# Optimization experiments

Hardware: AMD Instinct MI355X
Metric: run time of the kernel (lower is better)

The kernel has to match this reference:

```python
import jax, jax.numpy as jnp
import numpy as np

B, S, E = 2, 2048, 1024
H, NQ = 16, 8          # n_heads, n_qubits
D = E // H             # head_dim


def setup_inputs() -> dict:
    key = jax.random.key(0)
    ks = jax.random.split(key, 11)
    sc = 0.02
    return {
        "query": jax.random.normal(ks[0], (B, S, E), jnp.float32),
        "key":   jax.random.normal(ks[1], (B, S, E), jnp.float32),
        "value": jax.random.normal(ks[2], (B, S, E), jnp.float32),
        "Wq": jax.random.normal(ks[3], (E, NQ), jnp.float32) * sc,
        "bq": jnp.zeros((NQ,), jnp.float32),
        "Wk": jax.random.normal(ks[4], (E, NQ), jnp.float32) * sc,
        "bk": jnp.zeros((NQ,), jnp.float32),
        "Wv": jax.random.normal(ks[5], (E, E), jnp.float32) * sc,
        "bv": jnp.zeros((E,), jnp.float32),
        "Wo": jax.random.normal(ks[6], (E, E), jnp.float32) * sc,
        "bo": jnp.zeros((E,), jnp.float32),
    }


def reference(query, key, value, Wq, bq, Wk, bk, Wv, bv, Wo, bo):
    # Linear encoders (q/k are computed in the original but, because
    # _apply_rotation is the identity, they never influence the scores).
    q = query @ Wq + bq            # [B,S,NQ] (dead math, kept for fidelity)
    k = key @ Wk + bk              # [B,S,NQ]
    v = value @ Wv + bv            # [B,S,E]
    v = v.reshape(B, S, H, D).transpose(0, 2, 1, 3)  # [B,H,S,D]

    # Quantum overlap: both encoded states are always |0>, so
    # |<q_state|k_state>|^2 == 1 for every (b,i,j) pair.
    scores = jnp.full((B, H, S, S), 1.0 / np.sqrt(NQ), dtype=query.dtype)
    attn = jax.nn.softmax(scores, axis=-1)           # uniform 1/S weights

    out = jnp.einsum('bhij,bhjd->bhid', attn, v)     # [B,H,S,D]
    out = out.transpose(0, 2, 1, 3).reshape(B, S, E)
    out = out @ Wo + bo
    return out, attn
```

## Files before the change

kernel.cpp:

```cpp
#include <hip/hip_runtime.h>


typedef float floatx4 __attribute__((ext_vector_type(4)));

#define ATTN_BASE4 1048576LL
#define K1_FILLB   2512
#define K2_FILLB   2960
#define K3_FILLB   2720

__device__ __forceinline__ void fill_at(float* __restrict__ out, long long f4base) {
    floatx4* o4 = (floatx4*)out;
    const floatx4 av = (floatx4)(1.0f / 2048.0f);
    long long base = f4base + threadIdx.x;
    #pragma unroll
    for (int it = 0; it < 16; ++it)
        __builtin_nontemporal_store(av, &o4[base + it * 256]);
}

__global__ void __launch_bounds__(256)
k1_colsum_fill(const float* __restrict__ value,
               float* __restrict__ part1,
               float* __restrict__ out) {
    int blk = blockIdx.x, t = threadIdx.x;
    if (blk < 256) {
        int b = blk >> 7, sp = blk & 127;
        const floatx4* v4 = (const floatx4*)value;
        floatx4 acc = (floatx4)0.0f;
        int rowbase = b * 2048 + sp * 16;
        #pragma unroll
        for (int r = 0; r < 16; ++r)
            acc += v4[(size_t)(rowbase + r) * 256 + t];
        ((floatx4*)part1)[(size_t)(b * 128 + sp) * 256 + t] = acc;
    } else {
        fill_at(out, ATTN_BASE4 + (long long)(blk - 256) * 4096);
    }
}

__global__ void __launch_bounds__(256)
k2_z_fill(const float* __restrict__ part1,
          const float* __restrict__ Wv, const float* __restrict__ bv,
          float* __restrict__ z,
          float* __restrict__ out) {
    int blk = blockIdx.x, t = threadIdx.x;
    if (blk < 128) {
        __shared__ __align__(16) float vbar[1024];
        __shared__ float red[256];
        int b = blk >> 6, grp = blk & 63, e0 = grp * 16;

        const floatx4* p4 = (const floatx4*)part1 + (size_t)b * 128 * 256;
        floatx4 acc = (floatx4)0.0f;
        #pragma unroll 8
        for (int sp = 0; sp < 128; ++sp)
            acc += p4[sp * 256 + t];
        ((floatx4*)vbar)[t] = acc * (1.0f / 2048.0f);
        __syncthreads();

        int col = t & 15, seg = t >> 4;
        const float* wcol = Wv + e0 + col;
        float part = 0.f;
        int k0 = seg * 64;
        #pragma unroll 8
        for (int kk = 0; kk < 64; ++kk) {
            int k = k0 + kk;
            part += vbar[k] * wcol[(size_t)k * 1024];
        }
        red[t] = part;
        __syncthreads();
        if (t < 16) {
            float s = bv[e0 + t];
            #pragma unroll
            for (int g = 0; g < 16; ++g) s += red[g * 16 + t];
            z[b * 1024 + e0 + t] = s;
        }
    } else {
        fill_at(out, ATTN_BASE4 + (long long)K1_FILLB * 4096
                     + (long long)(blk - 128) * 4096);
    }
}

__global__ void __launch_bounds__(256)
k3_orow_bcast_fill(const float* __restrict__ z,
                   const float* __restrict__ Wo, const float* __restrict__ bo,
                   float* __restrict__ out) {
    int blk = blockIdx.x, t = threadIdx.x;
    if (blk < 128) {
        __shared__ __align__(16) float zsh[1024];
        __shared__ float red[256];
        __shared__ __align__(16) float orow[16];
        int b = blk >> 6, grp = blk & 63, e0 = grp * 16;

        ((floatx4*)zsh)[t] = ((const floatx4*)z)[b * 256 + t];
        __syncthreads();

        int col = t & 15, seg = t >> 4;
        const float* wcol = Wo + e0 + col;
        float part = 0.f;
        int k0 = seg * 64;
        #pragma unroll 8
        for (int kk = 0; kk < 64; ++kk) {
            int k = k0 + kk;
            part += zsh[k] * wcol[(size_t)k * 1024];
        }
        red[t] = part;
        __syncthreads();
        if (t < 16) {
            float s = bo[e0 + t];
            #pragma unroll
            for (int g = 0; g < 16; ++g) s += red[g * 16 + t];
            orow[t] = s;
        }
        __syncthreads();

        int q = t & 3, rl = t >> 2;
        floatx4 w = ((const floatx4*)orow)[q];
        floatx4* o4 = (floatx4*)out;
        size_t cbase = (size_t)(e0 >> 2) + q;
        #pragma unroll 4
        for (int r = rl; r < 2048; r += 64)
            __builtin_nontemporal_store(w, &o4[((size_t)b * 2048 + r) * 256 + cbase]);
    } else {
        fill_at(out, ATTN_BASE4 + (long long)(K1_FILLB + K2_FILLB) * 4096
                     + (long long)(blk - 128) * 4096);
    }
}

extern "C" void kernel_launch(void* const* d_in, const int* in_sizes, int n_in,
                              void* d_out, int out_size, void* d_ws, size_t ws_size,
                              hipStream_t stream) {
    const float* value = (const float*)d_in[2];
    const float* Wv    = (const float*)d_in[7];
    const float* bv    = (const float*)d_in[8];
    const float* Wo    = (const float*)d_in[9];
    const float* bo    = (const float*)d_in[10];
    float* out = (float*)d_out;

    float* part1 = (float*)d_ws;
    float* zbuf  = part1 + 262144;

    k1_colsum_fill    <<<256 + K1_FILLB, 256, 0, stream>>>(value, part1, out);
    k2_z_fill         <<<128 + K2_FILLB, 256, 0, stream>>>(part1, Wv, bv, zbuf, out);
    k3_orow_bcast_fill<<<128 + K3_FILLB, 256, 0, stream>>>(zbuf, Wo, bo, out);
}
```

Before: 114.1 us.

## Split Wv GEMV into partial-sum stage and widen Wo broadcast across more blocks

The v-bar @ Wv product is now split over k-slices into partial sums with coalesced float2 row reads of Wv, followed by a small reduction kernel that adds the bias. The Wo stage and its row broadcast run on 1024 blocks instead of 128, and every kernel uses a fixed 2048-block grid whose remaining blocks loop over 4 KB chunks of the uniform attention fill. The aim is to raise parallelism on the critical GEMV chain and keep the fill work balanced across stages. The cost is an extra kernel launch, an extra workspace round-trip, and the Wo GEMV being recomputed eight times per column group.

```diff
diff --git a/kernel.cpp b/kernel.cpp
--- a/kernel.cpp
+++ b/kernel.cpp
@@ -2,25 +2,33 @@
 
 
 typedef float floatx4 __attribute__((ext_vector_type(4)));
+typedef float floatx2 __attribute__((ext_vector_type(2)));
 
 #define ATTN_BASE4 1048576LL
-#define K1_FILLB   2512
-#define K2_FILLB   2960
-#define K3_FILLB   2720
+#define O1 0
+#define F1 7168
+#define O2 7168
+#define F2 8800
+#define O3 15968
+#define F3 9380
+#define O4 25348
+#define F4 7420
 
-__device__ __forceinline__ void fill_at(float* __restrict__ out, long long f4base) {
+__device__ __forceinline__ void fill_chunks(float* __restrict__ out,
+                                            int fb, int nf, int O, int F) {
     floatx4* o4 = (floatx4*)out;
     const floatx4 av = (floatx4)(1.0f / 2048.0f);
-    long long base = f4base + threadIdx.x;
-    #pragma unroll
-    for (int it = 0; it < 16; ++it)
-        __builtin_nontemporal_store(av, &o4[base + it * 256]);
+    for (int c = fb; c < F; c += nf) {
+        long long base = ATTN_BASE4 + ((long long)(O + c) << 10) + threadIdx.x;
+        #pragma unroll
+        for (int it = 0; it < 4; ++it)
+            __builtin_nontemporal_store(av, &o4[base + it * 256]);
+    }
 }
 
 __global__ void __launch_bounds__(256)
 k1_colsum_fill(const float* __restrict__ value,
-               float* __restrict__ part1,
-               float* __restrict__ out) {
+               float* __restrict__ part1, float* __restrict__ out) {
     int blk = blockIdx.x, t = threadIdx.x;
     if (blk < 256) {
         int b = blk >> 7, sp = blk & 127;
@@ -32,95 +40,107 @@
             acc += v4[(size_t)(rowbase + r) * 256 + t];
         ((floatx4*)part1)[(size_t)(b * 128 + sp) * 256 + t] = acc;
     } else {
-        fill_at(out, ATTN_BASE4 + (long long)(blk - 256) * 4096);
+        fill_chunks(out, blk - 256, 1792, O1, F1);
     }
 }
 
 __global__ void __launch_bounds__(256)
-k2_z_fill(const float* __restrict__ part1,
-          const float* __restrict__ Wv, const float* __restrict__ bv,
-          float* __restrict__ z,
-          float* __restrict__ out) {
+k2_zpart_fill(const float* __restrict__ part1, const float* __restrict__ Wv,
+              float* __restrict__ zpart, float* __restrict__ out) {
     int blk = blockIdx.x, t = threadIdx.x;
     if (blk < 128) {
-        __shared__ __align__(16) float vbar[1024];
         __shared__ float red[256];
-        int b = blk >> 6, grp = blk & 63, e0 = grp * 16;
+        __shared__ float vsl[32];
+        int b = blk >> 6, r = blk & 63, ks = r >> 1, eh = r & 1;
+        int k0 = ks * 32;
+        int kl = t & 31, sg = t >> 5;
+        float s = 0.f;
+        #pragma unroll
+        for (int i = 0; i < 16; ++i) {
+            int sp = sg * 16 + i;
+            s += part1[(size_t)(b * 128 + sp) * 1024 + k0 + kl];
+        }
+        red[t] = s;
+        __syncthreads();
+        if (t < 32) {
+            float v = 0.f;
+            #pragma unroll
+            for (int g = 0; g < 8; ++g) v += red[g * 32 + t];
+            vsl[t] = v * (1.0f / 2048.0f);
+        }
+        __syncthreads();
+        int e2 = eh * 512 + 2 * t;
+        floatx2 acc = (floatx2)0.0f;
+        #pragma unroll 8
+        for (int kk = 0; kk < 32; ++kk) {
+            floatx2 w = *(const floatx2*)&Wv[(size_t)(k0 + kk) * 1024 + e2];
+            acc += vsl[kk] * w;
+        }
+        *(floatx2*)&zpart[(size_t)(b * 32 + ks) * 1024 + e2] = acc;
+    } else {
+        fill_chunks(out, blk - 128, 1920, O2, F2);
+    }
+}
 
-        const floatx4* p4 = (const floatx4*)part1 + (size_t)b * 128 * 256;
-        floatx4 acc = (floatx4)0.0f;
+__global__ void __launch_bounds__(256)
+k3_zfin_fill(const float* __restrict__ zpart, const float* __restrict__ bv,
+             float* __restrict__ z, float* __restrict__ out) {
+    int blk = blockIdx.x, t = threadIdx.x;
+    if (blk < 64) {
+        int b = blk >> 5, es = blk & 31, e0 = es * 32;
+        if (t < 32) {
+            float s = bv[e0 + t];
+            #pragma unroll 8
+            for (int seg = 0; seg < 32; ++seg)
+                s += zpart[(size_t)(b * 32 + seg) * 1024 + e0 + t];
+            z[b * 1024 + e0 + t] = s;
+        }
+    } else {
+        fill_chunks(out, blk - 64, 1984, O3, F3);
+    }
+}
+
+__global__ void __launch_bounds__(256)
+k4_orow_bcast_fill(const float* __restrict__ z, const float* __restrict__ Wo,
+                   const float* __restrict__ bo, float* __restrict__ out) {
+    int blk = blockIdx.x, t = threadIdx.x;
+    if (blk < 1024) {
+        __shared__ __align__(16) float zsh[1024];
+        __shared__ float red[256];
+        __shared__ __align__(16) float orow[16];
+        int b = blk >> 9, r = blk & 511, cg = r >> 3, rr = r & 7;
+        int e0 = cg * 16;
+        ((floatx4*)zsh)[t] = ((const floatx4*)z)[b * 256 + t];
+        __syncthreads();
+        int eo = e0 + (t & 15), sg = t >> 4;
+        float part = 0.f;
+        int eb = sg * 64;
         #pragma unroll 8
-        for (int sp = 0; sp < 128; ++sp)
-            acc += p4[sp * 256 + t];
-        ((floatx4*)vbar)[t] = acc * (1.0f / 2048.0f);
-        __syncthreads();
-
-        int col = t & 15, seg = t >> 4;
-        const float* wcol = Wv + e0 + col;
-        float part = 0.f;
-        int k0 = seg * 64;
-        #pragma unroll 8
-        for (int kk = 0; kk < 64; ++kk) {
-            int k = k0 + kk;
-            part += vbar[k] * wcol[(size_t)k * 1024];
+        for (int ee = 0; ee < 64; ++ee) {
+            int e = eb + ee;
+            part += zsh[e] * Wo[(size_t)e * 1024 + eo];
         }
         red[t] = part;
         __syncthreads();
         if (t < 16) {
-            float s = bv[e0 + t];
+            float o = bo[e0 + t];
             #pragma unroll
-            for (int g = 0; g < 16; ++g) s += red[g * 16 + t];
-            z[b * 1024 + e0 + t] = s;
-        }
-    } else {
-        fill_at(out, ATTN_BASE4 + (long long)K1_FILLB * 4096
-                     + (long long)(blk - 128) * 4096);
-    }
-}
-
-__global__ void __launch_bounds__(256)
-k3_orow_bcast_fill(const float* __restrict__ z,
-                   const float* __restrict__ Wo, const float* __restrict__ bo,
-                   float* __restrict__ out) {
-    int blk = blockIdx.x, t = threadIdx.x;
-    if (blk < 128) {
-        __shared__ __align__(16) float zsh[1024];
-        __shared__ float red[256];
-        __shared__ __align__(16) float orow[16];
-        int b = blk >> 6, grp = blk & 63, e0 = grp * 16;
-
-        ((floatx4*)zsh)[t] = ((const floatx4*)z)[b * 256 + t];
-        __syncthreads();
-
-        int col = t & 15, seg = t >> 4;
-        const float* wcol = Wo + e0 + col;
-        float part = 0.f;
-        int k0 = seg * 64;
-        #pragma unroll 8
-        for (int kk = 0; kk < 64; ++kk) {
-            int k = k0 + kk;
-            part += zsh[k] * wcol[(size_t)k * 1024];
-        }
-        red[t] = part;
-        __syncthreads();
-        if (t < 16) {
-            float s = bo[e0 + t];
-            #pragma unroll
-            for (int g = 0; g < 16; ++g) s += red[g * 16 + t];
-            orow[t] = s;
+            for (int g = 0; g < 16; ++g) o += red[g * 16 + t];
+            orow[t] = o;
         }
         __syncthreads();
-
         int q = t & 3, rl = t >> 2;
         floatx4 w = ((const floatx4*)orow)[q];
         floatx4* o4 = (floatx4*)out;
-        size_t cbase = (size_t)(e0 >> 2) + q;
-        #pragma unroll 4
-        for (int r = rl; r < 2048; r += 64)
-            __builtin_nontemporal_store(w, &o4[((size_t)b * 2048 + r) * 256 + cbase]);
+        size_t cb = (size_t)(e0 >> 2) + q;
+        int rbase = rr * 256;
+        #pragma unroll
+        for (int i = 0; i < 4; ++i) {
+            int row = rbase + i * 64 + rl;
+            __builtin_nontemporal_store(w, &o4[((size_t)b * 2048 + row) * 256 + cb]);
+        }
     } else {
-        fill_at(out, ATTN_BASE4 + (long long)(K1_FILLB + K2_FILLB) * 4096
-                     + (long long)(blk - 128) * 4096);
+        fill_chunks(out, blk - 1024, 1024, O4, F4);
     }
 }
 
@@ -135,9 +155,11 @@
     float* out = (float*)d_out;
 
     float* part1 = (float*)d_ws;
-    float* zbuf  = part1 + 262144;
+    float* zpart = part1 + 262144;
+    float* zbuf  = zpart + 65536;
 
-    k1_colsum_fill    <<<256 + K1_FILLB, 256, 0, stream>>>(value, part1, out);
-    k2_z_fill         <<<128 + K2_FILLB, 256, 0, stream>>>(part1, Wv, bv, zbuf, out);
-    k3_orow_bcast_fill<<<128 + K3_FILLB, 256, 0, stream>>>(zbuf, Wo, bo, out);
+    k1_colsum_fill    <<<2048, 256, 0, stream>>>(value, part1, out);
+    k2_zpart_fill     <<<2048, 256, 0, stream>>>(part1, Wv, zpart, out);
+    k3_zfin_fill      <<<2048, 256, 0, stream>>>(zpart, bv, zbuf, out);
+    k4_orow_bcast_fill<<<2048, 256, 0, stream>>>(zbuf, Wo, bo, out);
 }
```

Result: faster. 109.2 us (-4.3%).
